# Performance work log

Measured on AMD Instinct MI355X. Metric: run time of the kernel, lower is better.

The kernel has to match this reference:

```python
import jax, jax.numpy as jnp
from jax import lax
import numpy as np


@jax.custom_vjp
def entmax15(x):
    return _entmax15_val(x)


def _entmax15_val(x):
    # 1.5-entmax along last axis (Peters et al. 2019), exact sort-based threshold
    x = (x - jnp.max(x, -1, keepdims=True)) / 2.0
    d = x.shape[-1]
    xs = -jnp.sort(-x, axis=-1)                      # descending
    rho = jnp.arange(1, d + 1, dtype=x.dtype)
    mean = jnp.cumsum(xs, -1) / rho
    mean_sq = jnp.cumsum(xs * xs, -1) / rho
    ss = rho * (mean_sq - mean * mean)
    delta = (1.0 - ss) / rho
    tau = mean - jnp.sqrt(jnp.clip(delta, 0.0))
    support = jnp.sum(tau <= xs, -1)
    tau_star = jnp.take_along_axis(tau, (support - 1)[..., None], -1)
    return jnp.square(jnp.clip(x - tau_star, 0.0))


def _entmax15_f(x):
    y = _entmax15_val(x)
    return y, y


def _entmax15_b(y, g):
    gppr = jnp.sqrt(y)                               # y^{2-alpha} with alpha=1.5
    dx = g * gppr
    q = jnp.sum(dx, -1, keepdims=True) / jnp.sum(gppr, -1, keepdims=True)
    return (dx - q * gppr,)


entmax15.defvjp(_entmax15_f, _entmax15_b)


def causal_conv(x, w, b, dilation):
    # x: [N, C_in, L]; left-pad (k-1)*dilation == conv+Chomp1d of the torch TCN
    pad = (w.shape[-1] - 1) * dilation
    y = lax.conv_general_dilated(x, w, (1,), [(pad, 0)], rhs_dilation=(dilation,),
                                 dimension_numbers=('NCH', 'OIH', 'NCH'))
    return y + b[None, :, None]


def temporal_block(x, w1, b1, w2, b2, wd, bd, dilation):
    h = jax.nn.relu(causal_conv(x, w1, b1, dilation))
    h = jax.nn.relu(causal_conv(h, w2, b2, dilation))
    res = x if wd is None else causal_conv(x, wd, bd, 1)  # 1x1 downsample
    return jax.nn.relu(h + res)


def _forward(src_seq, trg_seq,
             tcn0_w1, tcn0_b1, tcn0_w2, tcn0_b2, tcn0_wd, tcn0_bd,
             tcn1_w1, tcn1_b1, tcn1_w2, tcn1_b2,
             tcn2_w1, tcn2_b1, tcn2_w2, tcn2_b2,
             head1_w, head1_b, head2_w, head2_b):
    B, Ls, D = src_seq.shape
    Tp = trg_seq.shape[1]
    W = Ls + 1                                          # window = predict_start+1
    srctrg = jnp.concatenate([src_seq, trg_seq], axis=1)  # [B, Ls+Tp, D]
    # vectorized version of the python loop building in_conv (order: t-major, then batch)
    idx = jnp.arange(Tp)[:, None] + jnp.arange(W)[None, :]  # [Tp, W]
    win = srctrg[:, idx, :]                              # [B, Tp, W, D]
    x = win.transpose(1, 0, 3, 2).reshape(Tp * B, D, W)  # [N, D, W]
    x = temporal_block(x, tcn0_w1, tcn0_b1, tcn0_w2, tcn0_b2, tcn0_wd, tcn0_bd, 1)
    x = temporal_block(x, tcn1_w1, tcn1_b1, tcn1_w2, tcn1_b2, None, None, 2)
    x = temporal_block(x, tcn2_w1, tcn2_b1, tcn2_w2, tcn2_b2, None, None, 4)
    out = x.transpose(0, 2, 1)                           # [N, W, C]
    q = out[:, -1, :]                                    # [N, C]
    kv = out[:, :-1, :]                                  # [N, W-1, C]
    score = entmax15(jnp.einsum('nc,nlc->nl', q, kv))    # sparse attention weights
    c = jnp.einsum('nl,nlc->nc', score, kv)
    cc = jnp.concatenate([c, q], axis=-1)                # [N, 2C]
    y_hat = (cc @ head1_w.T + head1_b).reshape(Tp, B).T  # [B, Tp]
    sigma = jax.nn.softplus((cc @ head2_w.T + head2_b).reshape(Tp, B).T)
    return y_hat, sigma


def setup_inputs() -> dict:
    key = jax.random.key(0)
    ks = jax.random.split(key, 20)
    B, Ls, Tp, D, C, K = 128, 168, 24, 64, 128, 3
    n = lambda k, s: jax.random.normal(k, s, jnp.float32) * 0.05
    return {
        'src_seq': jax.random.normal(ks[0], (B, Ls, D), jnp.float32),
        'trg_seq': jax.random.normal(ks[1], (B, Tp, D), jnp.float32),
        'tcn0_w1': n(ks[2], (C, D, K)), 'tcn0_b1': n(ks[3], (C,)),
        'tcn0_w2': n(ks[4], (C, C, K)), 'tcn0_b2': n(ks[5], (C,)),
        'tcn0_wd': n(ks[6], (C, D, 1)), 'tcn0_bd': n(ks[7], (C,)),
        'tcn1_w1': n(ks[8], (C, C, K)), 'tcn1_b1': n(ks[9], (C,)),
        'tcn1_w2': n(ks[10], (C, C, K)), 'tcn1_b2': n(ks[11], (C,)),
        'tcn2_w1': n(ks[12], (C, C, K)), 'tcn2_b1': n(ks[13], (C,)),
        'tcn2_w2': n(ks[14], (C, C, K)), 'tcn2_b2': n(ks[15], (C,)),
        'head1_w': n(ks[16], (1, 2 * C)), 'head1_b': n(ks[17], (1,)),
        'head2_w': n(ks[18], (1, 2 * C)), 'head2_b': n(ks[19], (1,)),
    }


def reference(src_seq, trg_seq,
              tcn0_w1, tcn0_b1, tcn0_w2, tcn0_b2, tcn0_wd, tcn0_bd,
              tcn1_w1, tcn1_b1, tcn1_w2, tcn1_b2,
              tcn2_w1, tcn2_b1, tcn2_w2, tcn2_b2,
              head1_w, head1_b, head2_w, head2_b):
    return _forward(src_seq, trg_seq,
                    tcn0_w1, tcn0_b1, tcn0_w2, tcn0_b2, tcn0_wd, tcn0_bd,
                    tcn1_w1, tcn1_b1, tcn1_w2, tcn1_b2,
                    tcn2_w1, tcn2_b1, tcn2_w2, tcn2_b2,
                    head1_w, head1_b, head2_w, head2_b)
```

## Files before the change

### kernel.cpp

```cpp
#include <hip/hip_runtime.h>
#include <math.h>

typedef _Float16 f16;
typedef __attribute__((ext_vector_type(8))) _Float16 half8;
typedef __attribute__((ext_vector_type(4))) float f32x4;
typedef __attribute__((ext_vector_type(4))) float f4;

#define TPQ 24
#define BQ 128
#define LSQ 168

#define E0 0
#define ED 24576
#define E1 32768
#define E2 81920
#define E3 131072
#define E4 180224
#define E5 229376
#define WTOT 278528
#define OG2 278528
#define OG1 3424256
#define OG0 4276224

#define MFMA16(a, b, c) __builtin_amdgcn_mfma_f32_16x16x32_f16((a), (b), (c), 0, 0, 0)

extern "C" __global__ void pack_weights(
    const float* __restrict__ w01, const float* __restrict__ wd0,
    const float* __restrict__ w02, const float* __restrict__ w11,
    const float* __restrict__ w12, const float* __restrict__ w21,
    const float* __restrict__ w22, f16* __restrict__ ws)
{
    int e = blockIdx.x * 256 + threadIdx.x;
    if (e >= WTOT) return;
    const float* W; int CIN, KK, el;
    if (e < ED) { W = w01; CIN = 64; KK = 3; el = e; }
    else if (e < E1) { W = wd0; CIN = 64; KK = 1; el = e - ED; }
    else {
        int c = (e - E1) / 49152; el = (e - E1) % 49152; CIN = 128; KK = 3;
        W = (c == 0) ? w02 : (c == 1) ? w11 : (c == 2) ? w12 : (c == 3) ? w21 : w22;
    }
    const int KB = CIN / 32;
    const int frag = el >> 9, wi = el & 511, lane = wi >> 3, i = wi & 7;
    const int coT = frag / (KK * KB), rem = frag % (KK * KB);
    const int kk = rem / KB, kb = rem % KB;
    const int co = coT * 16 + (lane & 15);
    const int ci = kb * 32 + (lane >> 4) * 8 + i;
    ws[e] = (f16)W[(co * CIN + ci) * KK + kk];
}

template<int CIN, int KK, int DIL, int RES, int RELU>
__device__ __forceinline__ void phaseA(
    const char* __restrict__ inb, char* __restrict__ outb,
    const f16* __restrict__ ws, int eoff, const float* __restrict__ bias, int tid)
{
    constexpr int KB = CIN / 32;
    constexpr int RB = CIN * 2;
    const int lane = tid & 63, wid = tid >> 6;
    const int cg = wid & 3, wg = wid >> 2;
    const int colr = lane & 15, quad = lane >> 4;
    const half8* __restrict__ wp = (const half8*)(ws + eoff);
    half8 wf[2][KK][KB];
#pragma unroll
    for (int ct = 0; ct < 2; ++ct)
#pragma unroll
        for (int kk = 0; kk < KK; ++kk)
#pragma unroll
            for (int kb = 0; kb < KB; ++kb)
                wf[ct][kk][kb] = wp[((((cg * 2 + ct) * KK) + kk) * KB + kb) * 64 + lane];
    const float bv0 = bias[cg * 32 + colr], bv1 = bias[cg * 32 + 16 + colr];
    const int t0 = wg ? 3 : 0, t1 = wg ? 5 : 3;
    for (int t = t0; t < t1; ++t) {
        const int w = t * 16 + colr;
        f32x4 a0 = {0.f, 0.f, 0.f, 0.f}, a1 = {0.f, 0.f, 0.f, 0.f};
#pragma unroll
        for (int kk = 0; kk < KK; ++kk) {
            const int r8 = w + 8 - (KK - 1 - kk) * DIL;
            const int rb = r8 * RB, sx = r8 & 7;
#pragma unroll
            for (int kb = 0; kb < KB; ++kb) {
                const half8 a = *(const half8*)(inb + rb + ((((kb * 4 + quad) ^ sx)) << 4));
                a0 = MFMA16(a, wf[0][kk][kb], a0);
                a1 = MFMA16(a, wf[1][kk][kb], a1);
            }
        }
#pragma unroll
        for (int ct = 0; ct < 2; ++ct) {
            const float bv = ct ? bv1 : bv0;
            const int co = cg * 32 + ct * 16 + colr;
#pragma unroll
            for (int j = 0; j < 4; ++j) {
                const int r8o = t * 16 + quad * 4 + j + 8;
                char* p = outb + r8o * 256 + ((((co >> 3) ^ (r8o & 7))) << 4) + ((co & 7) << 1);
                float v = (ct ? a1[j] : a0[j]) + bv;
                if (RELU) v = fmaxf(v, 0.f);
                if (RES)  v = fmaxf(v + (float)*(const f16*)p, 0.f);
                *(f16*)p = (f16)v;
            }
        }
    }
}

extern "C" __global__ void __launch_bounds__(512, 4)
tcn_global(const float* __restrict__ src, const float* __restrict__ trg,
           f16* __restrict__ ws,
           const float* __restrict__ b01, const float* __restrict__ bd0,
           const float* __restrict__ b02, const float* __restrict__ b11,
           const float* __restrict__ b12, const float* __restrict__ b21,
           const float* __restrict__ b22)
{
    __shared__ __align__(16) char sX[88 * 128];
    __shared__ __align__(16) char sH1[88 * 256];
    __shared__ __align__(16) char sH2[88 * 256];
    const int tid = threadIdx.x;
    const int b = blockIdx.x >> 2, chunk = blockIdx.x & 3;
    const int u0 = chunk * 48;
    const float* srcb = src + (size_t)b * LSQ * 64;
    const float* trgb = trg + (size_t)b * TPQ * 64;

    for (int e = tid; e < 80 * 8; e += 512) {
        const int w = e >> 3, gg = e & 7;
        const int p = u0 - 28 + w;
        half8 v = {};
        if (p >= 0 && p < 192) {
            const float* ptr = (p < 168) ? (srcb + p * 64 + gg * 8) : (trgb + (p - 168) * 64 + gg * 8);
            const f4 f0 = *(const f4*)ptr; const f4 f1 = *(const f4*)(ptr + 4);
            v[0] = (f16)f0[0]; v[1] = (f16)f0[1]; v[2] = (f16)f0[2]; v[3] = (f16)f0[3];
            v[4] = (f16)f1[0]; v[5] = (f16)f1[1]; v[6] = (f16)f1[2]; v[7] = (f16)f1[3];
        }
        const int r8 = w + 8;
        *(half8*)(sX + r8 * 128 + ((gg ^ (r8 & 7)) << 4)) = v;
    }
    if (tid < 320) {
        const half8 z = {};
        if (tid < 64)       *(half8*)(sX + tid * 16) = z;
        else if (tid < 192) *(half8*)(sH1 + (tid - 64) * 16) = z;
        else                *(half8*)(sH2 + (tid - 192) * 16) = z;
    }
    __syncthreads();

    phaseA<64, 3, 1, 0, 1>(sX, sH1, ws, E0, b01, tid);
    phaseA<64, 1, 1, 0, 0>(sX, sH2, ws, ED, bd0, tid);
    __syncthreads();
    phaseA<128, 3, 1, 1, 1>(sH1, sH2, ws, E1, b02, tid);
    __syncthreads();
    phaseA<128, 3, 2, 0, 1>(sH2, sH1, ws, E2, b11, tid);
    if (chunk == 0) {
        for (int e = tid; e < 36 * 16; e += 512) {
            const int p = e >> 4, gc = e & 15, r8 = p + 36;
            const half8 v = *(const half8*)(sH2 + r8 * 256 + ((gc ^ (r8 & 7)) << 4));
            *(half8*)(ws + OG0 + (size_t)(b * 36 + p) * 128 + gc * 8) = v;
        }
    }
    __syncthreads();
    phaseA<128, 3, 2, 1, 1>(sH1, sH2, ws, E3, b12, tid);
    __syncthreads();
    phaseA<128, 3, 4, 0, 1>(sH2, sH1, ws, E4, b21, tid);
    if (chunk == 0) {
        for (int e = tid; e < 52 * 16; e += 512) {
            const int p = e >> 4, gc = e & 15, r8 = p + 36;
            const half8 v = *(const half8*)(sH2 + r8 * 256 + ((gc ^ (r8 & 7)) << 4));
            *(half8*)(ws + OG1 + (size_t)(b * 52 + p) * 128 + gc * 8) = v;
        }
    }
    __syncthreads();
    phaseA<128, 3, 4, 1, 1>(sH1, sH2, ws, E5, b22, tid);
    __syncthreads();
    for (int e = tid; e < 48 * 16; e += 512) {
        const int pl = e >> 4, gc = e & 15, r8 = pl + 36;
        const int p = u0 + pl;
        const half8 v = *(const half8*)(sH2 + r8 * 256 + ((gc ^ (r8 & 7)) << 4));
        *(half8*)(ws + OG2 + (size_t)(b * 192 + p) * 128 + gc * 8) = v;
    }
}

template<int CIN, int KK, int DIL, int WPG, int SIN, int SOUT, int RES, int RELU>
__device__ __forceinline__ void bc_conv(
    const char* __restrict__ inb, char* __restrict__ outb, const char* __restrict__ zrp,
    const f16* __restrict__ ws, int eoff, const float* __restrict__ bias, int tid)
{
    constexpr int KB = CIN / 32;
    constexpr int RB = CIN * 2;
    constexpr int NT = (4 * WPG) / 16;
    const int lane = tid & 63, wid = tid >> 6;
    const int colr = lane & 15, quad = lane >> 4;
    const half8* __restrict__ wp = (const half8*)(ws + eoff);
    half8 wf[2][KK][KB];
#pragma unroll
    for (int ct = 0; ct < 2; ++ct)
#pragma unroll
        for (int kk = 0; kk < KK; ++kk)
#pragma unroll
            for (int kb = 0; kb < KB; ++kb)
                wf[ct][kk][kb] = wp[((((wid * 2 + ct) * KK) + kk) * KB + kb) * 64 + lane];
    const float bv0 = bias[wid * 32 + colr], bv1 = bias[wid * 32 + 16 + colr];
    for (int t = 0; t < NT; ++t) {
        const int m = t * 16 + colr;
        const int g = m / WPG, w = m - g * WPG;
        f32x4 a0 = {0.f, 0.f, 0.f, 0.f}, a1 = {0.f, 0.f, 0.f, 0.f};
#pragma unroll
        for (int kk = 0; kk < KK; ++kk) {
            const int wq = w - (KK - 1 - kk) * DIL;
            const int row = g * SIN + wq;
            const char* rb = (wq < 0) ? zrp : (inb + row * RB);
            const int sx = (wq < 0) ? 0 : (row & 7);
#pragma unroll
            for (int kb = 0; kb < KB; ++kb) {
                const half8 a = *(const half8*)(rb + ((((kb * 4 + quad) ^ sx)) << 4));
                a0 = MFMA16(a, wf[0][kk][kb], a0);
                a1 = MFMA16(a, wf[1][kk][kb], a1);
            }
        }
#pragma unroll
        for (int ct = 0; ct < 2; ++ct) {
            const float bv = ct ? bv1 : bv0;
            const int co = wid * 32 + ct * 16 + colr;
#pragma unroll
            for (int j = 0; j < 4; ++j) {
                const int mo = t * 16 + quad * 4 + j;
                const int go = mo / WPG, wo = mo - go * WPG;
                const int row = go * SOUT + wo;
                char* p = outb + row * 256 + ((((co >> 3) ^ (row & 7))) << 4) + ((co & 7) << 1);
                float v = (ct ? a1[j] : a0[j]) + bv;
                if (RELU) v = fmaxf(v, 0.f);
                if (RES)  v = fmaxf(v + (float)*(const f16*)p, 0.f);
                *(f16*)p = (f16)v;
            }
        }
    }
}

__device__ __forceinline__ void bc_p2(
    const char* __restrict__ bx, const char* __restrict__ cb1, char* __restrict__ outB,
    const char* __restrict__ zrp, const f16* __restrict__ ws,
    const float* __restrict__ b02, const float* __restrict__ bd0, int tid)
{
    const int lane = tid & 63, wid = tid >> 6;
    const int colr = lane & 15, quad = lane >> 4;
    const half8* __restrict__ wpA = (const half8*)(ws + E1);
    const half8* __restrict__ wpD = (const half8*)(ws + ED);
    half8 wfa[2][3][4], wfd[2][2];
#pragma unroll
    for (int ct = 0; ct < 2; ++ct) {
#pragma unroll
        for (int kk = 0; kk < 3; ++kk)
#pragma unroll
            for (int kb = 0; kb < 4; ++kb)
                wfa[ct][kk][kb] = wpA[((((wid * 2 + ct) * 3) + kk) * 4 + kb) * 64 + lane];
#pragma unroll
        for (int kb = 0; kb < 2; ++kb)
            wfd[ct][kb] = wpD[((wid * 2 + ct) * 2 + kb) * 64 + lane];
    }
    const float ba0 = b02[wid * 32 + colr], ba1 = b02[wid * 32 + 16 + colr];
    const float bd0v = bd0[wid * 32 + colr], bd1v = bd0[wid * 32 + 16 + colr];
    const int m = colr;
    const int g = m >> 2, w = m & 3;
    f32x4 a0 = {0.f,0.f,0.f,0.f}, a1 = {0.f,0.f,0.f,0.f};
    f32x4 d0 = {0.f,0.f,0.f,0.f}, d1 = {0.f,0.f,0.f,0.f};
#pragma unroll
    for (int kk = 0; kk < 3; ++kk) {
        const int wq = w - (2 - kk);
        const int row = g * 4 + wq;
        const char* rb = (wq < 0) ? zrp : (cb1 + row * 256);
        const int sx = (wq < 0) ? 0 : (row & 7);
#pragma unroll
        for (int kb = 0; kb < 4; ++kb) {
            const half8 a = *(const half8*)(rb + ((((kb * 4 + quad) ^ sx)) << 4));
            a0 = MFMA16(a, wfa[0][kk][kb], a0);
            a1 = MFMA16(a, wfa[1][kk][kb], a1);
        }
    }
    {
        const int row = g * 4 + w;
        const char* rb = bx + row * 128;
        const int sx = row & 7;
#pragma unroll
        for (int kb = 0; kb < 2; ++kb) {
            const half8 x = *(const half8*)(rb + ((((kb * 4 + quad) ^ sx)) << 4));
            d0 = MFMA16(x, wfd[0][kb], d0);
            d1 = MFMA16(x, wfd[1][kb], d1);
        }
    }
#pragma unroll
    for (int ct = 0; ct < 2; ++ct) {
        const int co = wid * 32 + ct * 16 + colr;
#pragma unroll
        for (int j = 0; j < 4; ++j) {
            const int mo = quad * 4 + j;
            const int go = mo >> 2, wo = mo & 3;
            const int row = go * 28 + wo;
            char* p = outB + row * 256 + ((((co >> 3) ^ (row & 7))) << 4) + ((co & 7) << 1);
            const float ca = (ct ? a1[j] : a0[j]) + (ct ? ba1 : ba0);
            const float cd = (ct ? d1[j] : d0[j]) + (ct ? bd1v : bd0v);
            *(f16*)p = (f16)fmaxf(fmaxf(ca, 0.f) + cd, 0.f);
        }
    }
}

extern "C" __global__ void __launch_bounds__(256, 2)
tcn_bdattn(const float* __restrict__ src, const f16* __restrict__ ws,
           const float* __restrict__ b01, const float* __restrict__ bd0,
           const float* __restrict__ b02, const float* __restrict__ b11,
           const float* __restrict__ b12, const float* __restrict__ b21,
           const float* __restrict__ b22,
           const float* __restrict__ h1w, const float* __restrict__ h1b,
           const float* __restrict__ h2w, const float* __restrict__ h2b,
           float* __restrict__ out)
{
    __shared__ __align__(16) char BufB[112 * 256];
    __shared__ __align__(16) char BufC[112 * 256];
    __shared__ __align__(16) char sbx[16 * 128];
    __shared__ __align__(16) char scb1[16 * 256];
    __shared__ __align__(16) char zr[256];
    __shared__ float qf[512];
    __shared__ float sc[672];
    __shared__ float xs[672];
    __shared__ float taus[4];

    const int tid = threadIdx.x, lane = tid & 63, wid = tid >> 6;
    const int n0 = blockIdx.x << 2;
    const int tp = n0 >> 7, b0 = n0 & 127;

    if (tid < 16) *(half8*)(zr + tid * 16) = half8{};
    if (tid < 128) {
        const int g = tid >> 5, w = (tid >> 3) & 3, gg = tid & 7;
        const float* ptr = src + ((size_t)(b0 + g) * LSQ + (tp + w)) * 64 + gg * 8;
        const f4 f0 = *(const f4*)ptr; const f4 f1 = *(const f4*)(ptr + 4);
        half8 v;
        v[0] = (f16)f0[0]; v[1] = (f16)f0[1]; v[2] = (f16)f0[2]; v[3] = (f16)f0[3];
        v[4] = (f16)f1[0]; v[5] = (f16)f1[1]; v[6] = (f16)f1[2]; v[7] = (f16)f1[3];
        const int row = g * 4 + w;
        *(half8*)(sbx + row * 128 + ((gg ^ (row & 7)) << 4)) = v;
    }
    for (int e = tid; e < 512; e += 256) {
        const int g = e >> 7, pw = 4 + ((e >> 4) & 7), gc = e & 15;
        const half8 v = *(const half8*)(ws + OG0 + (size_t)((b0 + g) * 36 + (tp + pw)) * 128 + gc * 8);
        const int row = g * 28 + pw;
        *(half8*)(BufB + row * 256 + ((gc ^ (row & 7)) << 4)) = v;
    }
    for (int e = tid; e < 1024; e += 256) {
        const int g = e >> 8, pw = 12 + ((e >> 4) & 15), gc = e & 15;
        const half8 v = *(const half8*)(ws + OG1 + (size_t)((b0 + g) * 52 + (tp + pw)) * 128 + gc * 8);
        const int row = g * 28 + pw;
        *(half8*)(BufB + row * 256 + ((gc ^ (row & 7)) << 4)) = v;
    }
    for (int e = tid; e < 512; e += 256) {
        const int g = e >> 7, c = e & 127;
        qf[e] = (float)ws[OG2 + (size_t)((b0 + g) * 192 + tp + 168) * 128 + c];
    }
    __syncthreads();

    bc_conv<64, 3, 1, 4, 4, 4, 0, 1>(sbx, scb1, zr, ws, E0, b01, tid);
    __syncthreads();
    bc_p2(sbx, scb1, BufB, zr, ws, b02, bd0, tid);
    __syncthreads();
    bc_conv<128, 3, 2, 12, 28, 28, 0, 1>(BufB, BufC, zr, ws, E2, b11, tid);
    __syncthreads();
    bc_conv<128, 3, 2, 12, 28, 28, 1, 1>(BufC, BufB, zr, ws, E3, b12, tid);
    __syncthreads();
    bc_conv<128, 3, 4, 28, 28, 28, 0, 1>(BufB, BufC, zr, ws, E4, b21, tid);
    __syncthreads();
    bc_conv<128, 3, 4, 28, 28, 28, 1, 1>(BufC, BufB, zr, ws, E5, b22, tid);
    __syncthreads();

    const int g = wid;
    const int b = b0 + g;
    const f16* __restrict__ g2r = ws + OG2 + ((size_t)b * 192 + tp) * 128;

    for (int it = 0; it < 3; ++it) {
        const int w = it * 64 + lane;
        if (w < LSQ) {
            float s = 0.f;
            if (w < 28) {
                const int row = g * 28 + w, sx = row & 7;
                const char* rb = BufB + row * 256;
#pragma unroll
                for (int gc = 0; gc < 16; ++gc) {
                    const half8 kv = *(const half8*)(rb + ((gc ^ sx) << 4));
#pragma unroll
                    for (int j = 0; j < 8; ++j) s = fmaf((float)kv[j], qf[g * 128 + gc * 8 + j], s);
                }
            } else {
                const half8* rb = (const half8*)(g2r + (size_t)w * 128);
#pragma unroll
                for (int gc = 0; gc < 16; ++gc) {
                    const half8 kv = rb[gc];
#pragma unroll
                    for (int j = 0; j < 8; ++j) s = fmaf((float)kv[j], qf[g * 128 + gc * 8 + j], s);
                }
            }
            sc[g * 168 + w] = s;
        }
    }
    __syncthreads();

    const int i0 = lane * 3;
    {
        const float v0 = (i0 < LSQ) ? sc[g * 168 + i0] : 0.f;
        const float v1 = (i0 + 1 < LSQ) ? sc[g * 168 + i0 + 1] : 0.f;
        const float v2 = (i0 + 2 < LSQ) ? sc[g * 168 + i0 + 2] : 0.f;
        int r0 = 0, r1 = 0, r2 = 0;
        for (int m2 = 0; m2 < LSQ; ++m2) {
            const float u = sc[g * 168 + m2];
            r0 += (u > v0) || ((u == v0) && (m2 < i0));
            r1 += (u > v1) || ((u == v1) && (m2 < i0 + 1));
            r2 += (u > v2) || ((u == v2) && (m2 < i0 + 2));
        }
        if (i0 < LSQ)     xs[g * 168 + r0] = v0;
        if (i0 + 1 < LSQ) xs[g * 168 + r1] = v1;
        if (i0 + 2 < LSQ) xs[g * 168 + r2] = v2;
    }
    __syncthreads();

    {
        const float mx = xs[g * 168];
        const float a0 = (i0 < LSQ) ? (xs[g * 168 + i0] - mx) * 0.5f : 0.f;
        const float a1 = (i0 + 1 < LSQ) ? (xs[g * 168 + i0 + 1] - mx) * 0.5f : 0.f;
        const float a2 = (i0 + 2 < LSQ) ? (xs[g * 168 + i0 + 2] - mx) * 0.5f : 0.f;
        const float s1 = a0, s2 = a0 + a1, s3 = a0 + a1 + a2;
        const float q1 = a0 * a0, q2 = q1 + a1 * a1, q3 = q2 + a2 * a2;
        float ts = s3, tq = q3;
#pragma unroll
        for (int o = 1; o < 64; o <<= 1) {
            const float us = __shfl_up(ts, o);
            const float uq = __shfl_up(tq, o);
            if (lane >= o) { ts += us; tq += uq; }
        }
        const float eS = ts - s3, eQ = tq - q3;
        float tau0v, tau1v, tau2v; int ind = 0;
#define TAUC(CIDX, CS, CQ, AV, TVAR) { \
        const float rho = (float)(i0 + CIDX + 1); \
        const float mean = (CS) / rho; \
        const float msq = (CQ) / rho; \
        const float ssv = rho * (msq - mean * mean); \
        float delta = (1.f - ssv) / rho; \
        delta = delta > 0.f ? delta : 0.f; \
        TVAR = mean - sqrtf(delta); \
        if (i0 + CIDX < LSQ && TVAR <= (AV)) ++ind; }
        TAUC(0, eS + s1, eQ + q1, a0, tau0v)
        TAUC(1, eS + s2, eQ + q2, a1, tau1v)
        TAUC(2, eS + s3, eQ + q3, a2, tau2v)
#undef TAUC
#pragma unroll
        for (int o = 32; o; o >>= 1) ind += __shfl_xor(ind, o);
        const int sm1 = ind - 1;
        if (lane == sm1 / 3) {
            const int c = sm1 - (sm1 / 3) * 3;
            taus[g] = (c == 0) ? tau0v : (c == 1) ? tau1v : tau2v;
        }
    }
    __syncthreads();

    {
        const float mx = xs[g * 168];
        const float tau = taus[g];
        for (int it = 0; it < 3; ++it) {
            const int w = it * 64 + lane;
            if (w < LSQ) {
                float v = (sc[g * 168 + w] - mx) * 0.5f - tau;
                v = fmaxf(v, 0.f);
                sc[g * 168 + w] = v * v;
            }
        }
    }
    __syncthreads();

    {
        const int c0 = lane * 2;
        float cv0 = 0.f, cv1 = 0.f;
        for (int w = 0; w < LSQ; ++w) {
            const float pw = sc[g * 168 + w];
            float k0, k1;
            if (w < 28) {
                const int row = g * 28 + w, sx = row & 7;
                const char* p = BufB + row * 256 + (((c0 >> 3) ^ sx) << 4) + ((c0 & 7) << 1);
                k0 = (float)*(const f16*)p;
                k1 = (float)*(const f16*)(p + 2);
            } else {
                const f16* p = g2r + (size_t)w * 128 + c0;
                k0 = (float)p[0];
                k1 = (float)p[1];
            }
            cv0 = fmaf(pw, k0, cv0);
            cv1 = fmaf(pw, k1, cv1);
        }
        const float q0 = qf[g * 128 + c0], q1 = qf[g * 128 + c0 + 1];
        float s1 = h1w[c0] * cv0 + h1w[c0 + 1] * cv1 + h1w[128 + c0] * q0 + h1w[128 + c0 + 1] * q1;
        float s2 = h2w[c0] * cv0 + h2w[c0 + 1] * cv1 + h2w[128 + c0] * q0 + h2w[128 + c0 + 1] * q1;
#pragma unroll
        for (int o = 32; o; o >>= 1) {
            s1 += __shfl_xor(s1, o);
            s2 += __shfl_xor(s2, o);
        }
        if (lane == 0) {
            const float y1 = s1 + h1b[0];
            const float z = s2 + h2b[0];
            const float sp = (z > 0.f) ? (z + log1pf(expf(-z))) : log1pf(expf(z));
            out[b * TPQ + tp] = y1;
            out[BQ * TPQ + b * TPQ + tp] = sp;
        }
    }
}

extern "C" void kernel_launch(void* const* d_in, const int* in_sizes, int n_in,
                              void* d_out, int out_size, void* d_ws, size_t ws_size,
                              hipStream_t stream) {
    const float* src = (const float*)d_in[0];
    const float* trg = (const float*)d_in[1];
    const float* w01 = (const float*)d_in[2];
    const float* b01 = (const float*)d_in[3];
    const float* w02 = (const float*)d_in[4];
    const float* b02 = (const float*)d_in[5];
    const float* wd0 = (const float*)d_in[6];
    const float* bd0 = (const float*)d_in[7];
    const float* w11 = (const float*)d_in[8];
    const float* b11 = (const float*)d_in[9];
    const float* w12 = (const float*)d_in[10];
    const float* b12 = (const float*)d_in[11];
    const float* w21 = (const float*)d_in[12];
    const float* b21 = (const float*)d_in[13];
    const float* w22 = (const float*)d_in[14];
    const float* b22 = (const float*)d_in[15];
    const float* h1w = (const float*)d_in[16];
    const float* h1b = (const float*)d_in[17];
    const float* h2w = (const float*)d_in[18];
    const float* h2b = (const float*)d_in[19];
    f16* ws = (f16*)d_ws;

    pack_weights<<<dim3((WTOT + 255) / 256), dim3(256), 0, stream>>>(
        w01, wd0, w02, w11, w12, w21, w22, ws);

    tcn_global<<<dim3(BQ * 4), dim3(512), 0, stream>>>(
        src, trg, ws, b01, bd0, b02, b11, b12, b21, b22);

    tcn_bdattn<<<dim3(TPQ * BQ / 4), dim3(256), 0, stream>>>(
        src, ws, b01, bd0, b02, b11, b12, b21, b22,
        h1w, h1b, h2w, h2b, (float*)d_out);
}
```

Before: 168.0 us.

## Double tcn_bdattn block to 512 threads, one 16-channel tile per wave

The per-timestep attention kernel now runs 8 waves per block instead of 4. Each wave in the conv stages owns 16 output channels instead of 32, and accumulation is split across two MFMA chains. In the entmax/attention tail each group is split across two waves that each handle half the window, with partial sums reduced through shared memory. The tau broadcast now uses a shuffle instead of shared memory plus a barrier, and the normalization pass is fused into the weighted-sum loop. The aim is more parallelism and latency hiding, at the cost of an extra reduction barrier and higher occupancy demands from __launch_bounds__(512,4).

```diff
diff --git a/kernel.cpp b/kernel.cpp
--- a/kernel.cpp
+++ b/kernel.cpp
@@ -174,7 +174,7 @@
 }
 
 template<int CIN, int KK, int DIL, int WPG, int SIN, int SOUT, int RES, int RELU>
-__device__ __forceinline__ void bc_conv(
+__device__ __forceinline__ void bc_conv8(
     const char* __restrict__ inb, char* __restrict__ outb, const char* __restrict__ zrp,
     const f16* __restrict__ ws, int eoff, const float* __restrict__ bias, int tid)
 {
@@ -184,19 +184,18 @@
     const int lane = tid & 63, wid = tid >> 6;
     const int colr = lane & 15, quad = lane >> 4;
     const half8* __restrict__ wp = (const half8*)(ws + eoff);
-    half8 wf[2][KK][KB];
-#pragma unroll
-    for (int ct = 0; ct < 2; ++ct)
-#pragma unroll
-        for (int kk = 0; kk < KK; ++kk)
-#pragma unroll
-            for (int kb = 0; kb < KB; ++kb)
-                wf[ct][kk][kb] = wp[((((wid * 2 + ct) * KK) + kk) * KB + kb) * 64 + lane];
-    const float bv0 = bias[wid * 32 + colr], bv1 = bias[wid * 32 + 16 + colr];
+    half8 wf[KK][KB];
+#pragma unroll
+    for (int kk = 0; kk < KK; ++kk)
+#pragma unroll
+        for (int kb = 0; kb < KB; ++kb)
+            wf[kk][kb] = wp[((wid * KK + kk) * KB + kb) * 64 + lane];
+    const float bv = bias[wid * 16 + colr];
+#pragma unroll
     for (int t = 0; t < NT; ++t) {
         const int m = t * 16 + colr;
         const int g = m / WPG, w = m - g * WPG;
-        f32x4 a0 = {0.f, 0.f, 0.f, 0.f}, a1 = {0.f, 0.f, 0.f, 0.f};
+        f32x4 aA = {0.f, 0.f, 0.f, 0.f}, aB = {0.f, 0.f, 0.f, 0.f};
 #pragma unroll
         for (int kk = 0; kk < KK; ++kk) {
             const int wq = w - (KK - 1 - kk) * DIL;
@@ -206,30 +205,26 @@
 #pragma unroll
             for (int kb = 0; kb < KB; ++kb) {
                 const half8 a = *(const half8*)(rb + ((((kb * 4 + quad) ^ sx)) << 4));
-                a0 = MFMA16(a, wf[0][kk][kb], a0);
-                a1 = MFMA16(a, wf[1][kk][kb], a1);
+                if (kb & 1) aB = MFMA16(a, wf[kk][kb], aB);
+                else        aA = MFMA16(a, wf[kk][kb], aA);
             }
         }
-#pragma unroll
-        for (int ct = 0; ct < 2; ++ct) {
-            const float bv = ct ? bv1 : bv0;
-            const int co = wid * 32 + ct * 16 + colr;
-#pragma unroll
-            for (int j = 0; j < 4; ++j) {
-                const int mo = t * 16 + quad * 4 + j;
-                const int go = mo / WPG, wo = mo - go * WPG;
-                const int row = go * SOUT + wo;
-                char* p = outb + row * 256 + ((((co >> 3) ^ (row & 7))) << 4) + ((co & 7) << 1);
-                float v = (ct ? a1[j] : a0[j]) + bv;
-                if (RELU) v = fmaxf(v, 0.f);
-                if (RES)  v = fmaxf(v + (float)*(const f16*)p, 0.f);
-                *(f16*)p = (f16)v;
-            }
-        }
-    }
-}
-
-__device__ __forceinline__ void bc_p2(
+        const int co = wid * 16 + colr;
+#pragma unroll
+        for (int j = 0; j < 4; ++j) {
+            const int mo = t * 16 + quad * 4 + j;
+            const int go = mo / WPG, wo = mo - go * WPG;
+            const int row = go * SOUT + wo;
+            char* p = outb + row * 256 + ((((co >> 3) ^ (row & 7))) << 4) + ((co & 7) << 1);
+            float v = aA[j] + aB[j] + bv;
+            if (RELU) v = fmaxf(v, 0.f);
+            if (RES)  v = fmaxf(v + (float)*(const f16*)p, 0.f);
+            *(f16*)p = (f16)v;
+        }
+    }
+}
+
+__device__ __forceinline__ void bc_p2_8(
     const char* __restrict__ bx, const char* __restrict__ cb1, char* __restrict__ outB,
     const char* __restrict__ zrp, const f16* __restrict__ ws,
     const float* __restrict__ b02, const float* __restrict__ bd0, int tid)
@@ -238,24 +233,20 @@
     const int colr = lane & 15, quad = lane >> 4;
     const half8* __restrict__ wpA = (const half8*)(ws + E1);
     const half8* __restrict__ wpD = (const half8*)(ws + ED);
-    half8 wfa[2][3][4], wfd[2][2];
-#pragma unroll
-    for (int ct = 0; ct < 2; ++ct) {
-#pragma unroll
-        for (int kk = 0; kk < 3; ++kk)
-#pragma unroll
-            for (int kb = 0; kb < 4; ++kb)
-                wfa[ct][kk][kb] = wpA[((((wid * 2 + ct) * 3) + kk) * 4 + kb) * 64 + lane];
-#pragma unroll
-        for (int kb = 0; kb < 2; ++kb)
-            wfd[ct][kb] = wpD[((wid * 2 + ct) * 2 + kb) * 64 + lane];
-    }
-    const float ba0 = b02[wid * 32 + colr], ba1 = b02[wid * 32 + 16 + colr];
-    const float bd0v = bd0[wid * 32 + colr], bd1v = bd0[wid * 32 + 16 + colr];
-    const int m = colr;
-    const int g = m >> 2, w = m & 3;
-    f32x4 a0 = {0.f,0.f,0.f,0.f}, a1 = {0.f,0.f,0.f,0.f};
-    f32x4 d0 = {0.f,0.f,0.f,0.f}, d1 = {0.f,0.f,0.f,0.f};
+    half8 wfa[3][4], wfd[2];
+#pragma unroll
+    for (int kk = 0; kk < 3; ++kk)
+#pragma unroll
+        for (int kb = 0; kb < 4; ++kb)
+            wfa[kk][kb] = wpA[((wid * 3 + kk) * 4 + kb) * 64 + lane];
+#pragma unroll
+    for (int kb = 0; kb < 2; ++kb)
+        wfd[kb] = wpD[(wid * 2 + kb) * 64 + lane];
+    const float ba = b02[wid * 16 + colr];
+    const float bd = bd0[wid * 16 + colr];
+    const int g = colr >> 2, w = colr & 3;
+    f32x4 aA = {0.f,0.f,0.f,0.f}, aB = {0.f,0.f,0.f,0.f};
+    f32x4 dA = {0.f,0.f,0.f,0.f}, dB = {0.f,0.f,0.f,0.f};
 #pragma unroll
     for (int kk = 0; kk < 3; ++kk) {
         const int wq = w - (2 - kk);
@@ -265,38 +256,33 @@
 #pragma unroll
         for (int kb = 0; kb < 4; ++kb) {
             const half8 a = *(const half8*)(rb + ((((kb * 4 + quad) ^ sx)) << 4));
-            a0 = MFMA16(a, wfa[0][kk][kb], a0);
-            a1 = MFMA16(a, wfa[1][kk][kb], a1);
+            if (kb & 1) aB = MFMA16(a, wfa[kk][kb], aB);
+            else        aA = MFMA16(a, wfa[kk][kb], aA);
         }
     }
     {
         const int row = g * 4 + w;
         const char* rb = bx + row * 128;
         const int sx = row & 7;
-#pragma unroll
-        for (int kb = 0; kb < 2; ++kb) {
-            const half8 x = *(const half8*)(rb + ((((kb * 4 + quad) ^ sx)) << 4));
-            d0 = MFMA16(x, wfd[0][kb], d0);
-            d1 = MFMA16(x, wfd[1][kb], d1);
-        }
-    }
-#pragma unroll
-    for (int ct = 0; ct < 2; ++ct) {
-        const int co = wid * 32 + ct * 16 + colr;
-#pragma unroll
-        for (int j = 0; j < 4; ++j) {
-            const int mo = quad * 4 + j;
-            const int go = mo >> 2, wo = mo & 3;
-            const int row = go * 28 + wo;
-            char* p = outB + row * 256 + ((((co >> 3) ^ (row & 7))) << 4) + ((co & 7) << 1);
-            const float ca = (ct ? a1[j] : a0[j]) + (ct ? ba1 : ba0);
-            const float cd = (ct ? d1[j] : d0[j]) + (ct ? bd1v : bd0v);
-            *(f16*)p = (f16)fmaxf(fmaxf(ca, 0.f) + cd, 0.f);
-        }
-    }
-}
-
-extern "C" __global__ void __launch_bounds__(256, 2)
+        const half8 x0 = *(const half8*)(rb + (((0 * 4 + quad) ^ sx) << 4));
+        const half8 x1 = *(const half8*)(rb + (((1 * 4 + quad) ^ sx) << 4));
+        dA = MFMA16(x0, wfd[0], dA);
+        dB = MFMA16(x1, wfd[1], dB);
+    }
+    const int co = wid * 16 + colr;
+#pragma unroll
+    for (int j = 0; j < 4; ++j) {
+        const int mo = quad * 4 + j;
+        const int go = mo >> 2, wo = mo & 3;
+        const int row = go * 28 + wo;
+        char* p = outB + row * 256 + ((((co >> 3) ^ (row & 7))) << 4) + ((co & 7) << 1);
+        const float ca = aA[j] + aB[j] + ba;
+        const float cd = dA[j] + dB[j] + bd;
+        *(f16*)p = (f16)fmaxf(fmaxf(ca, 0.f) + cd, 0.f);
+    }
+}
+
+extern "C" __global__ void __launch_bounds__(512, 4)
 tcn_bdattn(const float* __restrict__ src, const f16* __restrict__ ws,
            const float* __restrict__ b01, const float* __restrict__ bd0,
            const float* __restrict__ b02, const float* __restrict__ b11,
@@ -314,7 +300,7 @@
     __shared__ float qf[512];
     __shared__ float sc[672];
     __shared__ float xs[672];
-    __shared__ float taus[4];
+    __shared__ float cvp[2][512];
 
     const int tid = threadIdx.x, lane = tid & 63, wid = tid >> 6;
     const int n0 = blockIdx.x << 2;
@@ -331,44 +317,49 @@
         const int row = g * 4 + w;
         *(half8*)(sbx + row * 128 + ((gg ^ (row & 7)) << 4)) = v;
     }
-    for (int e = tid; e < 512; e += 256) {
+    {
+        const int e = tid;
         const int g = e >> 7, pw = 4 + ((e >> 4) & 7), gc = e & 15;
         const half8 v = *(const half8*)(ws + OG0 + (size_t)((b0 + g) * 36 + (tp + pw)) * 128 + gc * 8);
         const int row = g * 28 + pw;
         *(half8*)(BufB + row * 256 + ((gc ^ (row & 7)) << 4)) = v;
     }
-    for (int e = tid; e < 1024; e += 256) {
+    for (int e = tid; e < 1024; e += 512) {
         const int g = e >> 8, pw = 12 + ((e >> 4) & 15), gc = e & 15;
         const half8 v = *(const half8*)(ws + OG1 + (size_t)((b0 + g) * 52 + (tp + pw)) * 128 + gc * 8);
         const int row = g * 28 + pw;
         *(half8*)(BufB + row * 256 + ((gc ^ (row & 7)) << 4)) = v;
     }
-    for (int e = tid; e < 512; e += 256) {
-        const int g = e >> 7, c = e & 127;
-        qf[e] = (float)ws[OG2 + (size_t)((b0 + g) * 192 + tp + 168) * 128 + c];
-    }
-    __syncthreads();
-
-    bc_conv<64, 3, 1, 4, 4, 4, 0, 1>(sbx, scb1, zr, ws, E0, b01, tid);
-    __syncthreads();
-    bc_p2(sbx, scb1, BufB, zr, ws, b02, bd0, tid);
-    __syncthreads();
-    bc_conv<128, 3, 2, 12, 28, 28, 0, 1>(BufB, BufC, zr, ws, E2, b11, tid);
-    __syncthreads();
-    bc_conv<128, 3, 2, 12, 28, 28, 1, 1>(BufC, BufB, zr, ws, E3, b12, tid);
-    __syncthreads();
-    bc_conv<128, 3, 4, 28, 28, 28, 0, 1>(BufB, BufC, zr, ws, E4, b21, tid);
-    __syncthreads();
-    bc_conv<128, 3, 4, 28, 28, 28, 1, 1>(BufC, BufB, zr, ws, E5, b22, tid);
-    __syncthreads();
-
-    const int g = wid;
+    if (tid < 64) {
+        const int g = tid >> 4, gc = tid & 15;
+        const half8 v = *(const half8*)(ws + OG2 + (size_t)((b0 + g) * 192 + tp + 168) * 128 + gc * 8);
+#pragma unroll
+        for (int j = 0; j < 8; ++j) qf[g * 128 + gc * 8 + j] = (float)v[j];
+    }
+    __syncthreads();
+
+    bc_conv8<64, 3, 1, 4, 4, 4, 0, 1>(sbx, scb1, zr, ws, E0, b01, tid);
+    __syncthreads();
+    bc_p2_8(sbx, scb1, BufB, zr, ws, b02, bd0, tid);
+    __syncthreads();
+    bc_conv8<128, 3, 2, 12, 28, 28, 0, 1>(BufB, BufC, zr, ws, E2, b11, tid);
+    __syncthreads();
+    bc_conv8<128, 3, 2, 12, 28, 28, 1, 1>(BufC, BufB, zr, ws, E3, b12, tid);
+    __syncthreads();
+    bc_conv8<128, 3, 4, 28, 28, 28, 0, 1>(BufB, BufC, zr, ws, E4, b21, tid);
+    __syncthreads();
+    bc_conv8<128, 3, 4, 28, 28, 28, 1, 1>(BufC, BufB, zr, ws, E5, b22, tid);
+    __syncthreads();
+
+    const int g = wid >> 1, h = wid & 1;
     const int b = b0 + g;
     const f16* __restrict__ g2r = ws + OG2 + ((size_t)b * 192 + tp) * 128;
-
-    for (int it = 0; it < 3; ++it) {
-        const int w = it * 64 + lane;
-        if (w < LSQ) {
+    const int wbase = h * 84;
+
+#pragma unroll
+    for (int it = 0; it < 2; ++it) {
+        const int w = wbase + it * 64 + lane;
+        if (it == 0 || lane < 20) {
             float s = 0.f;
             if (w < 28) {
                 const int row = g * 28 + w, sx = row & 7;
@@ -393,27 +384,27 @@
     }
     __syncthreads();
 
-    const int i0 = lane * 3;
     {
-        const float v0 = (i0 < LSQ) ? sc[g * 168 + i0] : 0.f;
-        const float v1 = (i0 + 1 < LSQ) ? sc[g * 168 + i0 + 1] : 0.f;
-        const float v2 = (i0 + 2 < LSQ) ? sc[g * 168 + i0 + 2] : 0.f;
-        int r0 = 0, r1 = 0, r2 = 0;
+        const int w0i = wbase + lane;
+        const int w1i = wbase + 64 + lane;
+        const float v0 = sc[g * 168 + w0i];
+        const float v1 = (lane < 20) ? sc[g * 168 + w1i] : 0.f;
+        int r0 = 0, r1 = 0;
         for (int m2 = 0; m2 < LSQ; ++m2) {
             const float u = sc[g * 168 + m2];
-            r0 += (u > v0) || ((u == v0) && (m2 < i0));
-            r1 += (u > v1) || ((u == v1) && (m2 < i0 + 1));
-            r2 += (u > v2) || ((u == v2) && (m2 < i0 + 2));
-        }
-        if (i0 < LSQ)     xs[g * 168 + r0] = v0;
-        if (i0 + 1 < LSQ) xs[g * 168 + r1] = v1;
-        if (i0 + 2 < LSQ) xs[g * 168 + r2] = v2;
-    }
-    __syncthreads();
-
+            r0 += (u > v0) || ((u == v0) && (m2 < w0i));
+            r1 += (u > v1) || ((u == v1) && (m2 < w1i));
+        }
+        xs[g * 168 + r0] = v0;
+        if (lane < 20) xs[g * 168 + r1] = v1;
+    }
+    __syncthreads();
+
+    const float mx = xs[g * 168];
+    float tau;
     {
-        const float mx = xs[g * 168];
-        const float a0 = (i0 < LSQ) ? (xs[g * 168 + i0] - mx) * 0.5f : 0.f;
+        const int i0 = lane * 3;
+        const float a0 = (i0     < LSQ) ? (xs[g * 168 + i0]     - mx) * 0.5f : 0.f;
         const float a1 = (i0 + 1 < LSQ) ? (xs[g * 168 + i0 + 1] - mx) * 0.5f : 0.f;
         const float a2 = (i0 + 2 < LSQ) ? (xs[g * 168 + i0 + 2] - mx) * 0.5f : 0.f;
         const float s1 = a0, s2 = a0 + a1, s3 = a0 + a1 + a2;
@@ -443,32 +434,20 @@
 #pragma unroll
         for (int o = 32; o; o >>= 1) ind += __shfl_xor(ind, o);
         const int sm1 = ind - 1;
-        if (lane == sm1 / 3) {
-            const int c = sm1 - (sm1 / 3) * 3;
-            taus[g] = (c == 0) ? tau0v : (c == 1) ? tau1v : tau2v;
-        }
-    }
-    __syncthreads();
-
-    {
-        const float mx = xs[g * 168];
-        const float tau = taus[g];
-        for (int it = 0; it < 3; ++it) {
-            const int w = it * 64 + lane;
-            if (w < LSQ) {
-                float v = (sc[g * 168 + w] - mx) * 0.5f - tau;
-                v = fmaxf(v, 0.f);
-                sc[g * 168 + w] = v * v;
-            }
-        }
-    }
-    __syncthreads();
+        const int srcl = sm1 / 3, c = sm1 - srcl * 3;
+        const float tsel = (c == 0) ? tau0v : (c == 1) ? tau1v : tau2v;
+        tau = __shfl(tsel, srcl);
+    }
 
     {
         const int c0 = lane * 2;
         float cv0 = 0.f, cv1 = 0.f;
-        for (int w = 0; w < LSQ; ++w) {
-            const float pw = sc[g * 168 + w];
+#pragma unroll 4
+        for (int wi = 0; wi < 84; ++wi) {
+            const int w = wbase + wi;
+            float pz = (sc[g * 168 + w] - mx) * 0.5f - tau;
+            pz = fmaxf(pz, 0.f);
+            const float pw = pz * pz;
             float k0, k1;
             if (w < 28) {
                 const int row = g * 28 + w, sx = row & 7;
@@ -483,9 +462,18 @@
             cv0 = fmaf(pw, k0, cv0);
             cv1 = fmaf(pw, k1, cv1);
         }
+        cvp[h][g * 128 + c0] = cv0;
+        cvp[h][g * 128 + c0 + 1] = cv1;
+    }
+    __syncthreads();
+
+    if (h == 0) {
+        const int c0 = lane * 2;
+        const float cva = cvp[0][g * 128 + c0]     + cvp[1][g * 128 + c0];
+        const float cvb = cvp[0][g * 128 + c0 + 1] + cvp[1][g * 128 + c0 + 1];
         const float q0 = qf[g * 128 + c0], q1 = qf[g * 128 + c0 + 1];
-        float s1 = h1w[c0] * cv0 + h1w[c0 + 1] * cv1 + h1w[128 + c0] * q0 + h1w[128 + c0 + 1] * q1;
-        float s2 = h2w[c0] * cv0 + h2w[c0 + 1] * cv1 + h2w[128 + c0] * q0 + h2w[128 + c0 + 1] * q1;
+        float s1 = h1w[c0] * cva + h1w[c0 + 1] * cvb + h1w[128 + c0] * q0 + h1w[128 + c0 + 1] * q1;
+        float s2 = h2w[c0] * cva + h2w[c0 + 1] * cvb + h2w[128 + c0] * q0 + h2w[128 + c0 + 1] * q1;
 #pragma unroll
         for (int o = 32; o; o >>= 1) {
             s1 += __shfl_xor(s1, o);
@@ -532,7 +520,7 @@
     tcn_global<<<dim3(BQ * 4), dim3(512), 0, stream>>>(
         src, trg, ws, b01, bd0, b02, b11, b12, b21, b22);
 
-    tcn_bdattn<<<dim3(TPQ * BQ / 4), dim3(256), 0, stream>>>(
+    tcn_bdattn<<<dim3(TPQ * BQ / 4), dim3(512), 0, stream>>>(
         src, ws, b01, bd0, b02, b11, b12, b21, b22,
         h1w, h1b, h2w, h2b, (float*)d_out);
 }
```

Result: slower. 182.6 us (+8.6%).
